# Kernel tuning notes

Hardware: AMD Instinct MI355X
Metric: run time of the kernel (lower is better)

## Reference

```python
import jax, jax.numpy as jnp
import numpy as np


def setup_inputs() -> dict:
    key = jax.random.key(0)
    k1, k2, k3 = jax.random.split(key, 3)
    B, C, H, W = 8, 512, 32, 32
    x = jax.random.normal(k1, (B, C, H, W), dtype=jnp.float32)
    # Conv2d(ch, ch, 3, 1, 1) weights, PyTorch OIHW layout
    fan_in = C * 3 * 3
    weight = jax.random.normal(k2, (C, C, 3, 3), dtype=jnp.float32) / np.sqrt(fan_in)
    bias = jax.random.normal(k3, (C,), dtype=jnp.float32) * 0.01
    return {"x": x, "weight": weight, "bias": bias}


def reference(x, weight, bias):
    up = jnp.repeat(jnp.repeat(x, 2, axis=2), 2, axis=3)
    # Conv3x3, stride 1, padding 1 (same spatial size)
    out = jax.lax.conv_general_dilated(
        up, weight,
        window_strides=(1, 1),
        padding=((1, 1), (1, 1)),
        dimension_numbers=("NCHW", "OIHW", "NCHW"),
    )
    return out + bias[None, :, None, None]
```

## Files before the change

kernel.cpp:

```cpp
#include <hip/hip_runtime.h>
#include <hip/hip_bf16.h>
#include <stdint.h>


typedef __attribute__((ext_vector_type(8)))  __bf16 bf16x8;
typedef __attribute__((ext_vector_type(4)))  float  f32x4;
typedef __attribute__((ext_vector_type(4)))  int    int4v;

__device__ __forceinline__ void async16(const void* g, void* l) {
  __builtin_amdgcn_global_load_lds(
      (const __attribute__((address_space(1))) void*)g,
      (__attribute__((address_space(3))) void*)l,
      16, 0, 0);
}

__global__ void prep_weff(const float* __restrict__ w,
                          __hip_bfloat16* __restrict__ weff) {
  const int idx = blockIdx.x * 256 + threadIdx.x;
  const int co = idx >> 9;
  const int ci = idx & 511;
  const float* wp = w + (size_t)idx * 9;
  float t[9];
#pragma unroll
  for (int i = 0; i < 9; ++i) t[i] = wp[i];
#pragma unroll
  for (int py = 0; py < 2; ++py) {
#pragma unroll
    for (int px = 0; px < 2; ++px) {
      const int p = py * 2 + px;
#pragma unroll
      for (int ky = 0; ky < 2; ++ky) {
        const int ulo = (ky == 0) ? 0 : (py == 0 ? 1 : 2);
        const int uhi = (ky == 0) ? (py == 0 ? 0 : 1) : 2;
#pragma unroll
        for (int kx = 0; kx < 2; ++kx) {
          const int vlo = (kx == 0) ? 0 : (px == 0 ? 1 : 2);
          const int vhi = (kx == 0) ? (px == 0 ? 0 : 1) : 2;
          float s = 0.f;
          for (int u = ulo; u <= uhi; ++u)
            for (int v = vlo; v <= vhi; ++v)
              s += t[u * 3 + v];
          const int kk = ky * 2 + kx;
          weff[(((size_t)p * 512 + co) * 4 + kk) * 512 + ci] = __float2bfloat16(s);
        }
      }
    }
  }
}

__global__ void prep_xpad(const float* __restrict__ x,
                          __hip_bfloat16* __restrict__ xpad) {
  const int blk = blockIdx.x;
  const int cib = blk & 7;
  const int r   = (blk >> 3) & 31;
  const int b   = blk >> 8;
  const int tid = threadIdx.x;
  __shared__ __align__(16) __hip_bfloat16 ldsT[32][80];
  const int ci_l = tid >> 2;
  const int wq   = tid & 3;
  const float* xp = x + (((size_t)(b * 512 + cib * 64 + ci_l) * 32 + r) * 32) + wq * 8;
  float4 v0 = *(const float4*)(xp);
  float4 v1 = *(const float4*)(xp + 4);
  const int wb = wq * 8;
  ldsT[wb + 0][ci_l] = __float2bfloat16(v0.x);
  ldsT[wb + 1][ci_l] = __float2bfloat16(v0.y);
  ldsT[wb + 2][ci_l] = __float2bfloat16(v0.z);
  ldsT[wb + 3][ci_l] = __float2bfloat16(v0.w);
  ldsT[wb + 4][ci_l] = __float2bfloat16(v1.x);
  ldsT[wb + 5][ci_l] = __float2bfloat16(v1.y);
  ldsT[wb + 6][ci_l] = __float2bfloat16(v1.z);
  ldsT[wb + 7][ci_l] = __float2bfloat16(v1.w);
  __syncthreads();
  const int w_o = tid >> 3;
  const int ch  = tid & 7;
  char* dst = (char*)xpad +
      ((((size_t)(b * 34 + (r + 1)) * 34) + (w_o + 1)) * 512 + cib * 64 + ch * 8) * 2;
  *(int4v*)dst = *(const int4v*)&ldsT[w_o][ch * 8];
}

#define MM(a, b, c) __builtin_amdgcn_mfma_f32_16x16x32_bf16((a), (b), (c), 0, 0, 0)
#define BAR() __builtin_amdgcn_s_barrier()
#define SCB() __builtin_amdgcn_sched_barrier(0)
#define PRIO(x) __builtin_amdgcn_s_setprio(x)
#define GATE(N) asm volatile("s_waitcnt vmcnt(" N ")" ::: "memory")

#define ST_A(T, h, d) do {                                                     \
    char* _l = lds + (d) * 32768 + (h) * 16384 + dA;                           \
    const __hip_bfloat16* _g = ((h) ? pA1 : pA0) + (size_t)(T) * 64;           \
    async16(_g, _l); async16(_g + 131072, _l + 8192); } while (0)

#define OFFB(T) (((((T) >> 4) * 34) + (((T) >> 3) & 1)) * 512 + ((T) & 7) * 64)
#define ST_B(T, h, d) do {                                                     \
    char* _l = lds + 65536 + (d) * 32768 + (h) * 16384 + dA;                   \
    const int _o = OFFB(T);                                                    \
    async16(((h) ? pB10 : pB00) + _o, _l);                                     \
    async16(((h) ? pB11 : pB01) + _o, _l + 8192); } while (0)

#define RD_A(D, S, mb) do {                                                    \
    _Pragma("unroll") for (int _m = 0; _m < 4; ++_m) {                         \
      (D)[_m * 2]     = *(const bf16x8*)((S) + ((mb) + _m) * 2048 + aoff0);    \
      (D)[_m * 2 + 1] = *(const bf16x8*)((S) + ((mb) + _m) * 2048 + aoff1); }  \
  } while (0)

#define RD_B(D, S, nb) do {                                                    \
    _Pragma("unroll") for (int _n = 0; _n < 2; ++_n) {                         \
      (D)[_n * 2]     = *(const bf16x8*)((S) + ((nb) + _n) * 2048 + aoff0);    \
      (D)[_n * 2 + 1] = *(const bf16x8*)((S) + ((nb) + _n) * 2048 + aoff1); }  \
  } while (0)

#define MFMAQ(mb, nb, A, B) do {                                               \
    _Pragma("unroll") for (int _m = 0; _m < 4; ++_m)                           \
      _Pragma("unroll") for (int _n = 0; _n < 2; ++_n) {                       \
        acc[(mb)+_m][(nb)+_n] = MM((A)[_m*2],   (B)[_n*2],   acc[(mb)+_m][(nb)+_n]); \
        acc[(mb)+_m][(nb)+_n] = MM((A)[_m*2+1], (B)[_n*2+1], acc[(mb)+_m][(nb)+_n]); } \
  } while (0)

#define ITER(T, SE, SM, S7, G3, G7) do {                                       \
   RD_A(A0, aS0, 0); RD_B(Bf, bS0, 0); if (SE) ST_A((T)+1, 1, 1);       \
    SCB(); BAR(); SCB(); PRIO(1); MFMAQ(0, 0, A0, Bf); PRIO(0); SCB(); BAR();  \
   RD_A(A1, aS0, 4); if (SE) ST_B((T)+1, 0, 1);                         \
    SCB(); BAR(); SCB(); PRIO(1); MFMAQ(4, 0, A1, Bf); PRIO(0); SCB(); BAR();  \
   RD_B(Bf, bS0, 2); if (SE) ST_B((T)+1, 1, 1);                         \
    SCB(); BAR(); SCB(); PRIO(1); MFMAQ(4, 2, A1, Bf); PRIO(0); SCB(); BAR();  \
   if (SM) ST_A((T)+2, 0, 0);                                           \
    SCB(); BAR(); SCB(); PRIO(1); MFMAQ(0, 2, A0, Bf); PRIO(0); SCB();         \
    GATE(G3); BAR();                                                           \
   RD_A(A0, aS1, 0); RD_B(Bf, bS1, 0); if (SM) ST_A((T)+2, 1, 0);       \
    SCB(); BAR(); SCB(); PRIO(1); MFMAQ(0, 0, A0, Bf); PRIO(0); SCB(); BAR();  \
   RD_A(A1, aS1, 4); if (SM) ST_B((T)+2, 0, 0);                         \
    SCB(); BAR(); SCB(); PRIO(1); MFMAQ(4, 0, A1, Bf); PRIO(0); SCB(); BAR();  \
   RD_B(Bf, bS1, 2); if (SM) ST_B((T)+2, 1, 0);                         \
    SCB(); BAR(); SCB(); PRIO(1); MFMAQ(4, 2, A1, Bf); PRIO(0); SCB(); BAR();  \
   if (S7) ST_A((T)+3, 0, 1);                                           \
    SCB(); BAR(); SCB(); PRIO(1); MFMAQ(0, 2, A0, Bf); PRIO(0); SCB();         \
    GATE(G7); BAR();                                                           \
} while (0)

__global__ __launch_bounds__(512, 2) void upconv_gemm(
    const __hip_bfloat16* __restrict__ xpad,
    const __hip_bfloat16* __restrict__ weff,
    const float* __restrict__ bias,
    float* __restrict__ out) {
  extern __shared__ __align__(16) char lds[];

  const int bid = blockIdx.x;
  const int g = bid & 7, i = bid >> 3;
  const int py = g >> 2;
  const int mt = (g >> 1) & 1;
  const int nh = g & 1;
  const int px = i & 1;
  const int nt = nh * 16 + (i >> 1);
  const int p  = py * 2 + px;
  const int co0 = mt << 8;
  const int n0  = nt << 8;
  const int b   = n0 >> 10;
  const int rb  = (n0 & 1023) >> 5;

  const int tid  = threadIdx.x;
  const int lane = tid & 63;
  const int wv   = tid >> 6;
  const int wr   = wv >> 2;
  const int wc   = wv & 3;

  const int srow = tid >> 3;
  const int sl   = (tid & 7) ^ (srow & 7);
  const int dA   = wv * 1024;

  const __hip_bfloat16* wpp = weff + ((size_t)p << 20);
  const __hip_bfloat16* pA0 = wpp + (size_t)(co0 + srow) * 2048 + sl * 8;
  const __hip_bfloat16* pA1 = pA0 + (size_t)128 * 2048;
  const __hip_bfloat16* pB00 = xpad +
      ((size_t)(b * 34 + rb + (srow >> 5) + py) * 34 + (srow & 31) + px) * 512 + sl * 8;
  const __hip_bfloat16* pB01 = xpad +
      ((size_t)(b * 34 + rb + ((64 + srow) >> 5) + py) * 34 + ((64 + srow) & 31) + px) * 512 + sl * 8;
  const __hip_bfloat16* pB10 = xpad +
      ((size_t)(b * 34 + rb + ((128 + srow) >> 5) + py) * 34 + ((128 + srow) & 31) + px) * 512 + sl * 8;
  const __hip_bfloat16* pB11 = xpad +
      ((size_t)(b * 34 + rb + ((192 + srow) >> 5) + py) * 34 + ((192 + srow) & 31) + px) * 512 + sl * 8;

  const int aoff0 = (lane & 15) * 128 + (((lane >> 4) ^ (lane & 7)) * 16);
  const int aoff1 = (lane & 15) * 128 + ((((lane >> 4) + 4) ^ (lane & 7)) * 16);
  const char* aS0 = lds + wr * 16384;
  const char* aS1 = aS0 + 32768;
  const char* bS0 = lds + 65536 + (wc >> 1) * 16384 + (wc & 1) * 8192;
  const char* bS1 = bS0 + 32768;

  f32x4 acc[8][4] = {};
  bf16x8 A0[8], A1[8], Bf[4];

  ST_A(0, 0, 0); ST_A(0, 1, 0); ST_B(0, 0, 0); ST_B(0, 1, 0);
  ST_A(1, 0, 1); ST_A(1, 1, 1); ST_B(1, 0, 1); ST_B(1, 1, 1);
  GATE("8"); BAR();

  ITER(0, false, true, true, "2", "2");
#pragma unroll 1
  for (int t = 2; t <= 28; t += 2) ITER(t, true, true, true, "2", "2");
  ITER(30, true, false, false, "0", "0");

#pragma unroll
  for (int m = 0; m < 8; ++m) {
    const int coB = co0 + wr * 128 + m * 16 + ((lane >> 4) << 2);
    float bv[4];
#pragma unroll
    for (int j = 0; j < 4; ++j) bv[j] = bias[coB + j];
#pragma unroll
    for (int nn = 0; nn < 4; ++nn) {
      const int nl = wc * 64 + nn * 16 + (lane & 15);
      const int rr = rb + (nl >> 5);
      const int ss = nl & 31;
      const int oh = rr * 2 + py;
      const int ow = ss * 2 + px;
      float* op = out + (((size_t)(b * 512 + coB) << 6) + oh) * 64 + ow;
#pragma unroll
      for (int j = 0; j < 4; ++j)
        op[(size_t)j * 4096] = acc[m][nn][j] + bv[j];
    }
  }
}

extern "C" void kernel_launch(void* const* d_in, const int* in_sizes, int n_in,
                              void* d_out, int out_size, void* d_ws, size_t ws_size,
                              hipStream_t stream) {
  (void)in_sizes; (void)n_in; (void)out_size; (void)ws_size;
  const float* x  = (const float*)d_in[0];
  const float* w  = (const float*)d_in[1];
  const float* bs = (const float*)d_in[2];
  float* out = (float*)d_out;
  char* ws = (char*)d_ws;
  __hip_bfloat16* xpad = (__hip_bfloat16*)ws;
  __hip_bfloat16* weff = (__hip_bfloat16*)(ws + (10u << 20));
  hipMemsetAsync(xpad, 0, (size_t)8 * 34 * 34 * 512 * 2, stream);
  prep_weff<<<dim3(1024), dim3(256), 0, stream>>>(w, weff);
  prep_xpad<<<dim3(2048), dim3(256), 0, stream>>>(x, xpad);
  upconv_gemm<<<dim3(256), dim3(512), 131072, stream>>>(xpad, weff, bs, out);
}
```

Baseline: 91.32 us.

## Restructure GEMM pipeline: stage B one tile ahead, A two ahead, explicit waits

Reorders the async global-to-LDS staging so B tiles are prefetched one K-step ahead and A tiles two ahead. Sched-barrier intrinsics are replaced with inline-asm s_barrier plus explicit lgkmcnt(0) waits. B fragments are split into two register sets, and the B source pointers are derived from a single base. The goal is to smooth memory latency hiding and reduce compiler scheduling constraints. It risks LDS hazards from the tighter B prefetch distance and more register pressure.

```diff
diff --git a/kernel.cpp b/kernel.cpp
--- a/kernel.cpp
+++ b/kernel.cpp
@@ -79,19 +79,19 @@
 }
 
 #define MM(a, b, c) __builtin_amdgcn_mfma_f32_16x16x32_bf16((a), (b), (c), 0, 0, 0)
-#define BAR() __builtin_amdgcn_s_barrier()
-#define SCB() __builtin_amdgcn_sched_barrier(0)
+#define BAR() asm volatile("s_barrier" ::: "memory")
+#define LGKM0() asm volatile("s_waitcnt lgkmcnt(0)" ::: "memory")
 #define PRIO(x) __builtin_amdgcn_s_setprio(x)
 #define GATE(N) asm volatile("s_waitcnt vmcnt(" N ")" ::: "memory")
 
-#define ST_A(T, h, d) do {                                                     \
-    char* _l = lds + (d) * 32768 + (h) * 16384 + dA;                           \
-    const __hip_bfloat16* _g = ((h) ? pA1 : pA0) + (size_t)(T) * 64;           \
+#define STH_A(T, h) do {                                                       \
+    char* _l = lds + ((T) & 1) * 32768 + (h) * 16384 + dA;                     \
+    const __hip_bfloat16* _g = pA0 + (size_t)(T) * 64 + (size_t)(h) * 262144;  \
     async16(_g, _l); async16(_g + 131072, _l + 8192); } while (0)
 
 #define OFFB(T) (((((T) >> 4) * 34) + (((T) >> 3) & 1)) * 512 + ((T) & 7) * 64)
-#define ST_B(T, h, d) do {                                                     \
-    char* _l = lds + 65536 + (d) * 32768 + (h) * 16384 + dA;                   \
+#define STH_B(T, h) do {                                                       \
+    char* _l = lds + 65536 + ((T) & 1) * 32768 + (h) * 16384 + dA;             \
     const int _o = OFFB(T);                                                    \
     async16(((h) ? pB10 : pB00) + _o, _l);                                     \
     async16(((h) ? pB11 : pB01) + _o, _l + 8192); } while (0)
@@ -115,25 +115,23 @@
         acc[(mb)+_m][(nb)+_n] = MM((A)[_m*2+1], (B)[_n*2+1], acc[(mb)+_m][(nb)+_n]); } \
   } while (0)
 
-#define ITER(T, SE, SM, S7, G3, G7) do {                                       \
-   RD_A(A0, aS0, 0); RD_B(Bf, bS0, 0); if (SE) ST_A((T)+1, 1, 1);       \
-    SCB(); BAR(); SCB(); PRIO(1); MFMAQ(0, 0, A0, Bf); PRIO(0); SCB(); BAR();  \
-   RD_A(A1, aS0, 4); if (SE) ST_B((T)+1, 0, 1);                         \
-    SCB(); BAR(); SCB(); PRIO(1); MFMAQ(4, 0, A1, Bf); PRIO(0); SCB(); BAR();  \
-   RD_B(Bf, bS0, 2); if (SE) ST_B((T)+1, 1, 1);                         \
-    SCB(); BAR(); SCB(); PRIO(1); MFMAQ(4, 2, A1, Bf); PRIO(0); SCB(); BAR();  \
-   if (SM) ST_A((T)+2, 0, 0);                                           \
-    SCB(); BAR(); SCB(); PRIO(1); MFMAQ(0, 2, A0, Bf); PRIO(0); SCB();         \
-    GATE(G3); BAR();                                                           \
-   RD_A(A0, aS1, 0); RD_B(Bf, bS1, 0); if (SM) ST_A((T)+2, 1, 0);       \
-    SCB(); BAR(); SCB(); PRIO(1); MFMAQ(0, 0, A0, Bf); PRIO(0); SCB(); BAR();  \
-   RD_A(A1, aS1, 4); if (SM) ST_B((T)+2, 0, 0);                         \
-    SCB(); BAR(); SCB(); PRIO(1); MFMAQ(4, 0, A1, Bf); PRIO(0); SCB(); BAR();  \
-   RD_B(Bf, bS1, 2); if (SM) ST_B((T)+2, 1, 0);                         \
-    SCB(); BAR(); SCB(); PRIO(1); MFMAQ(4, 2, A1, Bf); PRIO(0); SCB(); BAR();  \
-   if (S7) ST_A((T)+3, 0, 1);                                           \
-    SCB(); BAR(); SCB(); PRIO(1); MFMAQ(0, 2, A0, Bf); PRIO(0); SCB();         \
-    GATE(G7); BAR();                                                           \
+#define ITER(T, SE, SO, G1, G2) do {                                           \
+   RD_A(A0, aS0, 0); RD_B(B0, bS0, 0); STH_B((T) + 1, 0);             \
+    BAR(); LGKM0(); PRIO(1); MFMAQ(0, 0, A0, B0); PRIO(0); BAR();              \
+   RD_A(A1, aS0, 4); STH_B((T) + 1, 1);                               \
+    BAR(); LGKM0(); PRIO(1); MFMAQ(4, 0, A1, B0); PRIO(0); BAR();              \
+   RD_B(B1, bS0, 2); if (SE) STH_A((T) + 2, 0);                       \
+    BAR(); LGKM0(); PRIO(1); MFMAQ(4, 2, A1, B1); PRIO(0); BAR();              \
+   if (SE) STH_A((T) + 2, 1);                                         \
+    BAR(); PRIO(1); MFMAQ(0, 2, A0, B1); PRIO(0); GATE(G1); BAR();             \
+   RD_A(A0, aS1, 0); RD_B(B0, bS1, 0); if (SE) STH_B((T) + 2, 0);     \
+    BAR(); LGKM0(); PRIO(1); MFMAQ(0, 0, A0, B0); PRIO(0); BAR();              \
+   RD_A(A1, aS1, 4); if (SE) STH_B((T) + 2, 1);                       \
+    BAR(); LGKM0(); PRIO(1); MFMAQ(4, 0, A1, B0); PRIO(0); BAR();              \
+   RD_B(B1, bS1, 2); if (SO) STH_A((T) + 3, 0);                       \
+    BAR(); LGKM0(); PRIO(1); MFMAQ(4, 2, A1, B1); PRIO(0); BAR();              \
+   if (SO) STH_A((T) + 3, 1);                                         \
+    BAR(); PRIO(1); MFMAQ(0, 2, A0, B1); PRIO(0); GATE(G2); BAR();             \
 } while (0)
 
 __global__ __launch_bounds__(512, 2) void upconv_gemm(
@@ -168,15 +166,11 @@
 
   const __hip_bfloat16* wpp = weff + ((size_t)p << 20);
   const __hip_bfloat16* pA0 = wpp + (size_t)(co0 + srow) * 2048 + sl * 8;
-  const __hip_bfloat16* pA1 = pA0 + (size_t)128 * 2048;
   const __hip_bfloat16* pB00 = xpad +
       ((size_t)(b * 34 + rb + (srow >> 5) + py) * 34 + (srow & 31) + px) * 512 + sl * 8;
-  const __hip_bfloat16* pB01 = xpad +
-      ((size_t)(b * 34 + rb + ((64 + srow) >> 5) + py) * 34 + ((64 + srow) & 31) + px) * 512 + sl * 8;
-  const __hip_bfloat16* pB10 = xpad +
-      ((size_t)(b * 34 + rb + ((128 + srow) >> 5) + py) * 34 + ((128 + srow) & 31) + px) * 512 + sl * 8;
-  const __hip_bfloat16* pB11 = xpad +
-      ((size_t)(b * 34 + rb + ((192 + srow) >> 5) + py) * 34 + ((192 + srow) & 31) + px) * 512 + sl * 8;
+  const __hip_bfloat16* pB01 = pB00 + (size_t)2 * 34 * 512;
+  const __hip_bfloat16* pB10 = pB00 + (size_t)4 * 34 * 512;
+  const __hip_bfloat16* pB11 = pB00 + (size_t)6 * 34 * 512;
 
   const int aoff0 = (lane & 15) * 128 + (((lane >> 4) ^ (lane & 7)) * 16);
   const int aoff1 = (lane & 15) * 128 + ((((lane >> 4) + 4) ^ (lane & 7)) * 16);
@@ -186,16 +180,15 @@
   const char* bS1 = bS0 + 32768;
 
   f32x4 acc[8][4] = {};
-  bf16x8 A0[8], A1[8], Bf[4];
-
-  ST_A(0, 0, 0); ST_A(0, 1, 0); ST_B(0, 0, 0); ST_B(0, 1, 0);
-  ST_A(1, 0, 1); ST_A(1, 1, 1); ST_B(1, 0, 1); ST_B(1, 1, 1);
-  GATE("8"); BAR();
-
-  ITER(0, false, true, true, "2", "2");
+  bf16x8 A0[8], A1[8], B0[4], B1[4];
+
+  STH_A(0, 0); STH_A(0, 1); STH_B(0, 0); STH_B(0, 1);
+  STH_A(1, 0); STH_A(1, 1);
+  GATE("4"); BAR();
+
 #pragma unroll 1
-  for (int t = 2; t <= 28; t += 2) ITER(t, true, true, true, "2", "2");
-  ITER(30, true, false, false, "0", "0");
+  for (int t = 0; t <= 28; t += 2) ITER(t, true, true, "4", "4");
+  ITER(30, false, false, "0", "0");
 
 #pragma unroll
   for (int m = 0; m < 8; ++m) {
```

Result: faster. 86.06 us (-5.8%).
